# Performance work log

Measured on AMD Instinct MI355X. Metric: run time of the kernel, lower is better.

## Reference

```python
import jax, jax.numpy as jnp
import numpy as np

# YOLOv5-style NMS + scale_coords constants
CONF_THRES = 0.25
IOU_THRES = 0.45
MAX_DET = 300      # max detections kept per image
TOPK = 1024        # candidate pool fed to greedy NMS (static for jit)
MAX_WH = 4096.0    # class offset for class-aware NMS
IMG1 = (640.0, 640.0)   # shape1: letterboxed network input (h, w)
IMG0 = (720.0, 1280.0)  # shape0: original image (h, w)


def xywh2xyxy(x):
    xy, wh = x[..., :2], x[..., 2:4] * 0.5
    return jnp.concatenate([xy - wh, xy + wh], axis=-1)


def iou_one_to_many(b, B):
    # b: [4], B: [K,4] in xyxy
    lt = jnp.maximum(b[:2], B[:, :2])
    rb = jnp.minimum(b[2:], B[:, 2:])
    wh = jnp.clip(rb - lt, 0.0)
    inter = wh[:, 0] * wh[:, 1]
    a1 = (b[2] - b[0]) * (b[3] - b[1])
    a2 = (B[:, 2] - B[:, 0]) * (B[:, 3] - B[:, 1])
    return inter / (a1 + a2 - inter + 1e-9)


def nms_single(pred):
    # pred: [N, 85] = xywh, obj, 80 class scores
    obj = pred[:, 4]
    conf_all = obj[:, None] * pred[:, 5:]          # obj * cls conf
    conf = conf_all.max(axis=-1)
    cls = jnp.argmax(conf_all, axis=-1).astype(pred.dtype)
    boxes = xywh2xyxy(pred[:, :4])
    valid = (obj > CONF_THRES) & (conf > CONF_THRES)
    sc = jnp.where(valid, conf, -1.0)
    sc_top, idx = jax.lax.top_k(sc, TOPK)          # candidate pool
    b = boxes[idx]                                  # [K,4]
    c = cls[idx]                                    # [K]
    off = b + c[:, None] * MAX_WH                   # class-aware offset boxes

    def body(i, state):
        s, sel, selv = state
        p = jnp.argmax(s)
        pv = s[p] > 0.0
        iou = iou_one_to_many(off[p], off)
        s = jnp.where(iou > IOU_THRES, -1.0, s).at[p].set(-1.0)
        return s, sel.at[i].set(p), selv.at[i].set(pv)

    init = (sc_top, jnp.zeros(MAX_DET, jnp.int32), jnp.zeros(MAX_DET, bool))
    _, sel, selv = jax.lax.fori_loop(0, MAX_DET, body, init)

    det = jnp.concatenate(
        [b[sel], sc_top[sel][:, None], c[sel][:, None]], axis=-1)  # [max_det,6]
    return jnp.where(selv[:, None], det, 0.0)


def scale_coords(coords):
    # undo letterbox: IMG1 (h1,w1) -> IMG0 (h0,w0)
    h1, w1 = IMG1
    h0, w0 = IMG0
    gain = min(h1 / h0, w1 / w0)
    pad_x = (w1 - w0 * gain) / 2.0
    pad_y = (h1 - h0 * gain) / 2.0
    x1 = jnp.clip((coords[..., 0] - pad_x) / gain, 0.0, w0)
    y1 = jnp.clip((coords[..., 1] - pad_y) / gain, 0.0, h0)
    x2 = jnp.clip((coords[..., 2] - pad_x) / gain, 0.0, w0)
    y2 = jnp.clip((coords[..., 3] - pad_y) / gain, 0.0, h0)
    return jnp.stack([x1, y1, x2, y2], axis=-1)


def setup_inputs() -> dict:
    key = jax.random.key(0)
    kxy, kwh, kobj, kcls = jax.random.split(key, 4)
    B, N, NC = 16, 25200, 80
    xy = jax.random.uniform(kxy, (B, N, 2), jnp.float32) * 640.0
    wh = jax.random.uniform(kwh, (B, N, 2), jnp.float32) * 160.0 + 2.0
    obj = jax.random.uniform(kobj, (B, N, 1), jnp.float32)
    cls = jax.random.uniform(kcls, (B, N, NC), jnp.float32)
    pred = jnp.concatenate([xy, wh, obj, cls], axis=-1)  # [B, N, 85]
    return {"pred": pred}


def reference(pred):
    det = jax.vmap(nms_single)(pred)                 # [B, max_det, 6]
    boxes = scale_coords(det[..., :4])
    # columns: x1,y1,x2,y2 (rescaled), score, label
    return jnp.concatenate([boxes, det[..., 4:]], axis=-1)
```

## Files before the change

kernel.cpp:

```cpp
#include <hip/hip_runtime.h>
#include <stdint.h>

#define N_CAND 25200
#define NB 16
#define ROW 85
#define TK 1024
#define MAXDET 300
#define CAP 2048
#define BITS_LO 0x3E800000u

typedef unsigned long long u64;
typedef unsigned int u32;

static __device__ __forceinline__ u64 u64min(u64 a, u64 b) { return a < b ? a : b; }
static __device__ __forceinline__ u64 u64max(u64 a, u64 b) { return a > b ? a : b; }

__global__ __launch_bounds__(256) void score_kernel(const float* __restrict__ pred,
                                                    u64* __restrict__ keys)
{
#pragma clang fp contract(off)
    __shared__ float tile[64 * ROW];
    const int tid = threadIdx.x;
    const int row0 = blockIdx.x * 64;
    const float4* src = (const float4*)(pred + (size_t)row0 * ROW);
    float4* dst = (float4*)tile;
#pragma unroll
    for (int i = 0; i < 6; ++i) {
        int idx = tid + (i << 8);
        if (idx < (64 * ROW) / 4) dst[idx] = src[idx];
    }
    __syncthreads();

    const int r = tid >> 2, sub = tid & 3;
    const float* rowp = tile + r * ROW;
    const float obj = rowp[4];
    const int base = 5 + sub * 20;
    float bv = obj * rowp[base];
    int bi = base - 5;
#pragma unroll
    for (int c = 1; c < 20; ++c) {
        float p = obj * rowp[base + c];
        if (p > bv) { bv = p; bi = base - 5 + c; }
    }
#pragma unroll
    for (int off = 1; off <= 2; off <<= 1) {
        float ov = __shfl_xor(bv, off, 64);
        int   oi = __shfl_xor(bi, off, 64);
        if (ov > bv || (ov == bv && oi < bi)) { bv = ov; bi = oi; }
    }
    if (sub == 0) {
        int w = row0 + r;
        u32 n = (u32)(w % N_CAND);
        u64 key = 0;
        if (obj > 0.25f && bv > 0.25f)
            key = ((u64)__float_as_uint(bv) << 32) | (((u64)(25199u - n)) << 7) | (u32)bi;
        keys[w] = key;
    }
}

__global__ __launch_bounds__(1024) void topk_kernel(const float* __restrict__ pred,
                                                    const u64* __restrict__ keys,
                                                    float4* __restrict__ soaA,
                                                    float4* __restrict__ soaB)
{
#pragma clang fp contract(off)
    __shared__ u64 sbuf[CAP];
    __shared__ u32 histA[2048];
    __shared__ u32 histB[2048];
    __shared__ u32 s_t;
    __shared__ int s_cnt;

    const int tid = threadIdx.x;
    const int b = blockIdx.x;
    const u64* kb = keys + (size_t)b * N_CAND;
    const float* pb = pred + (size_t)b * N_CAND * ROW;

    for (int i = tid; i < 2048; i += 1024) histA[i] = 0;
    if (tid == 0) { s_cnt = 0; s_t = 0; }
    __syncthreads();

    for (int n = tid; n < N_CAND; n += 1024) {
        u32 bits = (u32)(kb[n] >> 32);
        if (bits) {
            int bin = (int)((bits - BITS_LO) >> 13);
            bin = bin < 0 ? 0 : (bin > 2047 ? 2047 : bin);
            atomicAdd(&histA[bin], 1u);
        }
    }
    __syncthreads();

    u32* srcp = histA; u32* dstp = histB;
    for (int step = 1; step < 2048; step <<= 1) {
        for (int i = tid; i < 2048; i += 1024)
            dstp[i] = srcp[i] + ((i + step < 2048) ? srcp[i + step] : 0u);
        __syncthreads();
        u32* t = srcp; srcp = dstp; dstp = t;
    }
    for (int i = tid; i < 2048; i += 1024) {
        u32 S = srcp[i];
        if (S >= TK && (i == 2047 || srcp[i + 1] < TK)) s_t = (u32)i;
    }
    __syncthreads();
    const u32 thr = BITS_LO + (s_t << 13);

    for (int n = tid; n < N_CAND; n += 1024) {
        u64 k = kb[n];
        if ((u32)(k >> 32) >= thr) {
            int pos = atomicAdd(&s_cnt, 1);
            if (pos < CAP) sbuf[pos] = k;
        }
    }
    __syncthreads();
    int cnt = s_cnt; if (cnt > CAP) cnt = CAP;
    for (int i = tid; i < CAP; i += 1024) if (i >= cnt) sbuf[i] = 0ull;
    __syncthreads();

    {
        const int E0 = tid << 1;
        u64 e0 = sbuf[E0], e1 = sbuf[E0 + 1];
        for (int k = 2; k <= CAP; k <<= 1) {
            for (int j = k >> 1; j > 0; j >>= 1) {
                const bool asc = ((E0 & k) == 0);
                if (j >= 128) {
                    __syncthreads();
                    sbuf[E0] = e0; sbuf[E0 + 1] = e1;
                    __syncthreads();
                    u64 p0 = sbuf[E0 ^ j], p1 = sbuf[(E0 + 1) ^ j];
                    const bool low = ((E0 & j) == 0);
                    e0 = (asc == low) ? u64min(e0, p0) : u64max(e0, p0);
                    e1 = (asc == low) ? u64min(e1, p1) : u64max(e1, p1);
                } else if (j >= 2) {
                    const int l = j >> 1;
                    u64 p0 = __shfl_xor(e0, l, 64);
                    u64 p1 = __shfl_xor(e1, l, 64);
                    const bool low = ((E0 & j) == 0);
                    e0 = (asc == low) ? u64min(e0, p0) : u64max(e0, p0);
                    e1 = (asc == low) ? u64min(e1, p1) : u64max(e1, p1);
                } else {
                    u64 mn = u64min(e0, e1), mx = u64max(e0, e1);
                    e0 = asc ? mn : mx;
                    e1 = asc ? mx : mn;
                }
            }
        }
        __syncthreads();
        sbuf[E0] = e0; sbuf[E0 + 1] = e1;
        __syncthreads();
    }

    {
        const int i = tid;
        u64 k = sbuf[CAP - 1 - i];
        u32 bits = (u32)(k >> 32);
        float4 A, Bv;
        if (bits) {
            u32 lo = (u32)k;
            u32 n = 25199u - (lo >> 7);
            float c = (float)(lo & 127u);
            const float* rp = pb + (size_t)n * ROW;
            float x = rp[0], y = rp[1], ww = rp[2], hh = rp[3];
            float hw = ww * 0.5f, hv = hh * 0.5f;
            float x1 = x - hw, y1 = y - hv, x2 = x + hw, y2 = y + hv;
            float offc = c * 4096.0f;
            float area = ((x2 + offc) - (x1 + offc)) * ((y2 + offc) - (y1 + offc));
            A = make_float4(x1, y1, x2, y2);
            Bv = make_float4(area, __uint_as_float(bits), c, 0.0f);
        } else {
            A = make_float4(0.0f, 0.0f, 0.0f, 0.0f);
            Bv = make_float4(0.0f, -1.0f, 0.0f, 0.0f);
        }
        soaA[b * TK + i] = A;
        soaB[b * TK + i] = Bv;
    }
}

__global__ __launch_bounds__(512) void mask_kernel(const float4* __restrict__ soaA,
                                                   const float4* __restrict__ soaB,
                                                   u64* __restrict__ masks)
{
#pragma clang fp contract(off)
    __shared__ float4 cA[TK];
    __shared__ float4 cB[TK];
    const int tid = threadIdx.x;
    const int b = blockIdx.y;
    const int rbase = blockIdx.x * 64;
    for (int i = tid; i < TK; i += 512) { cA[i] = soaA[b * TK + i]; cB[i] = soaB[b * TK + i]; }
    __syncthreads();

    const int wave = tid >> 6, lane = tid & 63;
    for (int rr = 0; rr < 8; ++rr) {
        int i = rbase + (wave << 3) + rr;
        float4 P = cA[i]; float4 Pb = cB[i];
        float offp = Pb.z * 4096.0f;
        float px1 = P.x + offp, py1 = P.y + offp, px2 = P.z + offp, py2 = P.w + offp;
        float parea = Pb.x;
        u64 myword = 0;
        for (int word = 0; word < 16; ++word) {
            int j = (word << 6) + lane;
            float4 Q = cA[j]; float4 Qb = cB[j];
            float offj = Qb.z * 4096.0f;
            float qx1 = Q.x + offj, qy1 = Q.y + offj, qx2 = Q.z + offj, qy2 = Q.w + offj;
            float ltx = fmaxf(px1, qx1), lty = fmaxf(py1, qy1);
            float rbx = fminf(px2, qx2), rby = fminf(py2, qy2);
            float w2 = fmaxf(rbx - ltx, 0.0f), h2 = fmaxf(rby - lty, 0.0f);
            float inter = w2 * h2;
            float iou = inter / (parea + Qb.x - inter + 1e-9f);
            u64 m = __ballot(iou > 0.45f);
            if (lane == word) myword = m;
        }
        if (lane < 16) masks[((size_t)(b * TK + i) << 4) + lane] = myword;
    }
}

__global__ __launch_bounds__(64) void sweep_kernel(const float4* __restrict__ soaA,
                                                   const float4* __restrict__ soaB,
                                                   const u64* __restrict__ masks,
                                                   float* __restrict__ out)
{
#pragma clang fp contract(off)
    __shared__ int sel[MAXDET];
    const int lane = threadIdx.x;
    const int b = blockIdx.x;
    const u64* mb = masks + ((size_t)(b * TK) << 4);

    int nv = TK;
    for (int k = 0; k < 16; ++k) {
        float s = soaB[b * TK + (k << 6) + lane].y;
        u64 m = __ballot(s > 0.0f);
        if (m != ~0ull) { nv = (k << 6) + (int)__builtin_ctzll(~m); break; }
    }

    u64 removed = 0;
    int nsel = 0;
    bool done = (nv == 0);
    const int li = lane & 15;

    u64 cur[8], nxt[8];
#pragma unroll
    for (int r = 0; r < 8; ++r) cur[r] = mb[((size_t)r << 4) + li];

    for (int c = 0; c < 128 && !done; ++c) {
        int nb0 = (c + 1) << 3;
#pragma unroll
        for (int r = 0; r < 8; ++r) {
            int i2 = nb0 + r; if (i2 > TK - 1) i2 = TK - 1;
            nxt[r] = mb[((size_t)i2 << 4) + li];
        }
#pragma unroll
        for (int r = 0; r < 8; ++r) {
            int i = (c << 3) + r;
            if (!done && i < nv) {
                u64 wv = __shfl(removed, i >> 6, 64);
                if (!((wv >> (i & 63)) & 1ull)) {
                    if (lane == 0) sel[nsel] = i;
                    removed |= cur[r];
                    ++nsel;
                    if (nsel == MAXDET) done = true;
                }
            } else if (i >= nv) done = true;
        }
#pragma unroll
        for (int r = 0; r < 8; ++r) cur[r] = nxt[r];
    }
    __syncthreads();

    for (int r = lane; r < MAXDET; r += 64) {
        float* o = out + ((size_t)b * MAXDET + r) * 6;
        if (r < nsel) {
            int p = sel[r];
            float4 A = soaA[b * TK + p];
            float4 Bv = soaB[b * TK + p];
            float X1 = (A.x - 0.0f) / 0.5f;
            float Y1 = (A.y - 140.0f) / 0.5f;
            float X2 = (A.z - 0.0f) / 0.5f;
            float Y2 = (A.w - 140.0f) / 0.5f;
            X1 = fminf(fmaxf(X1, 0.0f), 1280.0f);
            Y1 = fminf(fmaxf(Y1, 0.0f), 720.0f);
            X2 = fminf(fmaxf(X2, 0.0f), 1280.0f);
            Y2 = fminf(fmaxf(Y2, 0.0f), 720.0f);
            o[0] = X1; o[1] = Y1; o[2] = X2; o[3] = Y2;
            o[4] = Bv.y; o[5] = Bv.z;
        } else {
            o[0] = 0.0f; o[1] = 0.0f; o[2] = 0.0f;
            o[3] = 0.0f; o[4] = 0.0f; o[5] = 0.0f;
        }
    }
}

extern "C" void kernel_launch(void* const* d_in, const int* in_sizes, int n_in,
                              void* d_out, int out_size, void* d_ws, size_t ws_size,
                              hipStream_t stream)
{
    const float* pred = (const float*)d_in[0];
    float* out = (float*)d_out;

    u64* keys = (u64*)d_ws;
    u64* masks = (u64*)d_ws;
    float4* soaA = (float4*)((char*)d_ws + 3225600);
    float4* soaB = (float4*)((char*)d_ws + 3225600 + 262144);

    score_kernel<<<(NB * N_CAND) / 64, 256, 0, stream>>>(pred, keys);
    topk_kernel<<<NB, 1024, 0, stream>>>(pred, keys, soaA, soaB);
    mask_kernel<<<dim3(16, NB), 512, 0, stream>>>(soaA, soaB, masks);
    sweep_kernel<<<NB, 64, 0, stream>>>(soaA, soaB, masks, out);
}
```

Baseline: 120.4 us.

## Build score histogram in score kernel and use diagonal-block NMS sweep

```diff
diff --git a/kernel.cpp b/kernel.cpp
--- a/kernel.cpp
+++ b/kernel.cpp
@@ -15,8 +15,9 @@
 static __device__ __forceinline__ u64 u64min(u64 a, u64 b) { return a < b ? a : b; }
 static __device__ __forceinline__ u64 u64max(u64 a, u64 b) { return a > b ? a : b; }
 
-__global__ __launch_bounds__(256) void score_kernel(const float* __restrict__ pred,
-                                                    u64* __restrict__ keys)
+__global__ __launch_bounds__(256, 8) void score_kernel(const float* __restrict__ pred,
+                                                       u64* __restrict__ keys,
+                                                       u32* __restrict__ ghist)
 {
 #pragma clang fp contract(off)
     __shared__ float tile[64 * ROW];
@@ -50,16 +51,23 @@
     }
     if (sub == 0) {
         int w = row0 + r;
-        u32 n = (u32)(w % N_CAND);
+        u32 b = (u32)w / N_CAND;
+        u32 n = (u32)w - b * N_CAND;
         u64 key = 0;
-        if (obj > 0.25f && bv > 0.25f)
-            key = ((u64)__float_as_uint(bv) << 32) | (((u64)(25199u - n)) << 7) | (u32)bi;
+        if (obj > 0.25f && bv > 0.25f) {
+            u32 bits = __float_as_uint(bv);
+            key = ((u64)bits << 32) | (((u64)(25199u - n)) << 7) | (u32)bi;
+            int bin = (int)((bits - BITS_LO) >> 13);
+            bin = bin < 0 ? 0 : (bin > 2047 ? 2047 : bin);
+            atomicAdd(&ghist[(b << 11) + (u32)bin], 1u);
+        }
         keys[w] = key;
     }
 }
 
 __global__ __launch_bounds__(1024) void topk_kernel(const float* __restrict__ pred,
                                                     const u64* __restrict__ keys,
+                                                    const u32* __restrict__ ghist,
                                                     float4* __restrict__ soaA,
                                                     float4* __restrict__ soaB)
 {
@@ -75,18 +83,8 @@
     const u64* kb = keys + (size_t)b * N_CAND;
     const float* pb = pred + (size_t)b * N_CAND * ROW;
 
-    for (int i = tid; i < 2048; i += 1024) histA[i] = 0;
+    for (int i = tid; i < 2048; i += 1024) histA[i] = ghist[(b << 11) + i];
     if (tid == 0) { s_cnt = 0; s_t = 0; }
-    __syncthreads();
-
-    for (int n = tid; n < N_CAND; n += 1024) {
-        u32 bits = (u32)(kb[n] >> 32);
-        if (bits) {
-            int bin = (int)((bits - BITS_LO) >> 13);
-            bin = bin < 0 ? 0 : (bin > 2047 ? 2047 : bin);
-            atomicAdd(&histA[bin], 1u);
-        }
-    }
     __syncthreads();
 
     u32* srcp = histA; u32* dstp = histB;
@@ -232,35 +230,31 @@
 
     u64 removed = 0;
     int nsel = 0;
-    bool done = (nv == 0);
-    const int li = lane & 15;
-
-    u64 cur[8], nxt[8];
-#pragma unroll
-    for (int r = 0; r < 8; ++r) cur[r] = mb[((size_t)r << 4) + li];
-
-    for (int c = 0; c < 128 && !done; ++c) {
-        int nb0 = (c + 1) << 3;
-#pragma unroll
-        for (int r = 0; r < 8; ++r) {
-            int i2 = nb0 + r; if (i2 > TK - 1) i2 = TK - 1;
-            nxt[r] = mb[((size_t)i2 << 4) + li];
-        }
-#pragma unroll
-        for (int r = 0; r < 8; ++r) {
-            int i = (c << 3) + r;
-            if (!done && i < nv) {
-                u64 wv = __shfl(removed, i >> 6, 64);
-                if (!((wv >> (i & 63)) & 1ull)) {
-                    if (lane == 0) sel[nsel] = i;
-                    removed |= cur[r];
-                    ++nsel;
-                    if (nsel == MAXDET) done = true;
-                }
-            } else if (i >= nv) done = true;
-        }
-#pragma unroll
-        for (int r = 0; r < 8; ++r) cur[r] = nxt[r];
+    u64 diag = mb[((size_t)lane << 4)];
+    for (int w = 0; w < 16; ++w) {
+        u64 dnext = (w < 15) ? mb[((size_t)(((w + 1) << 6) + lane) << 4) + (w + 1)] : 0ull;
+        u64 wv = __shfl(removed, w, 64);
+        int rem = nv - (w << 6);
+        u64 validm = (rem >= 64) ? ~0ull : ((rem <= 0) ? 0ull : ((1ull << rem) - 1ull));
+        u64 alive = validm & ~wv;
+        u64 selbits = 0;
+        while (alive != 0ull && nsel < MAXDET) {
+            int i = (int)__builtin_ctzll(alive);
+            if (lane == 0) sel[nsel] = (w << 6) + i;
+            ++nsel;
+            selbits |= (1ull << i);
+            u64 d = __shfl(diag, i, 64);
+            alive &= ~d;
+            alive &= ~(1ull << i);
+        }
+        u64 sb = selbits;
+        while (sb != 0ull) {
+            int i = (int)__builtin_ctzll(sb);
+            sb &= sb - 1ull;
+            if (lane < 16) removed |= mb[((size_t)((w << 6) + i) << 4) + lane];
+        }
+        diag = dnext;
+        if (nsel >= MAXDET || rem <= 64) break;
     }
     __syncthreads();
 
@@ -298,9 +292,11 @@
     u64* masks = (u64*)d_ws;
     float4* soaA = (float4*)((char*)d_ws + 3225600);
     float4* soaB = (float4*)((char*)d_ws + 3225600 + 262144);
-
-    score_kernel<<<(NB * N_CAND) / 64, 256, 0, stream>>>(pred, keys);
-    topk_kernel<<<NB, 1024, 0, stream>>>(pred, keys, soaA, soaB);
+    u32* ghist = (u32*)((char*)d_ws + 3749888);
+
+    hipMemsetAsync(ghist, 0, NB * 2048 * sizeof(u32), stream);
+    score_kernel<<<(NB * N_CAND) / 64, 256, 0, stream>>>(pred, keys, ghist);
+    topk_kernel<<<NB, 1024, 0, stream>>>(pred, keys, ghist, soaA, soaB);
     mask_kernel<<<dim3(16, NB), 512, 0, stream>>>(soaA, soaB, masks);
     sweep_kernel<<<NB, 64, 0, stream>>>(soaA, soaB, masks, out);
 }
```

Result: slower. 167.7 us (+39.3%).
